# Kernel tuning notes

Measured on AMD Instinct MI355X. Metric: run time of the kernel, lower is better.

## Reference

```python
import jax, jax.numpy as jnp
import numpy as np

S_LEN, BATCH, D, HK, M, L, VOCAB = 1024, 4, 1024, 1024, 4096, 6, 32000
EPS = 1e-5


def layernorm(x, g, b):
    mu = x.mean(-1, keepdims=True)
    xc = x - mu
    var = (xc * xc).mean(-1, keepdims=True)
    return xc * jax.lax.rsqrt(var + EPS) * g + b


def block(z, wq, wk, wv, wc, g1, bb1, w1, b1, w2, b2, g2, bb2):
    # Faithful to the torch block: permute (1,0,2) at entry, never permute back.
    x = jnp.swapaxes(z, 0, 1)  # [B', S', d]
    d = x.shape[-1]
    Q = jnp.einsum('bsd,ed->bse', x, wq)
    K = jnp.einsum('bsd,ed->bse', x, wk)
    V = jnp.einsum('bsd,ed->bse', x, wv)
    # NOTE: scale is sqrt(embed_dim)=sqrt(d), not sqrt(k); no causal mask (faithful).
    scores = jnp.einsum('bse,bte->bst', Q, K) / jnp.sqrt(jnp.asarray(d, x.dtype))
    A = jax.nn.softmax(scores, axis=-1)
    ctx = jnp.einsum('bst,bte->bse', A, V)
    att = jnp.einsum('bse,de->bsd', ctx, wc) + x
    h = layernorm(att, g1, bb1)
    # NOTE: no nonlinearity in the FFN (faithful to the source).
    f = jnp.einsum('bsd,md->bsm', h, w1) + b1
    f = jnp.einsum('bsm,dm->bsd', f, w2) + b2
    return layernorm(f + h, g2, bb2)


def forward(x, word_emb, pos_emb, wq, wk, wv, wc, ln1_g, ln1_b, w1, b1, w2, b2,
            ln2_g, ln2_b, dec_w, dec_b, out_bias):
    S = x.shape[0]
    z = word_emb[x] * jnp.sqrt(jnp.asarray(D, word_emb.dtype))  # [S,B,d]
    z = jax.nn.relu(z + pos_emb[jnp.arange(S)][:, None, :])
    for i in range(L):  # small fixed layer count; shapes alternate layout so no scan
        z = block(z, wq[i], wk[i], wv[i], wc[i], ln1_g[i], ln1_b[i],
                  w1[i], b1[i], w2[i], b2[i], ln2_g[i], ln2_b[i])
    logits = jnp.einsum('sbd,vd->sbv', z, dec_w) + dec_b + out_bias
    return jax.nn.log_softmax(logits, axis=-1)


def setup_inputs() -> dict:
    key = jax.random.key(0)
    ks = jax.random.split(key, 16)
    std = jnp.float32(0.02)
    return {
        'x': jax.random.randint(ks[0], (S_LEN, BATCH), 0, VOCAB),
        'word_emb': jax.random.normal(ks[1], (VOCAB, D), jnp.float32) * std,
        'pos_emb': jax.random.normal(ks[2], (S_LEN, D), jnp.float32) * std,
        'wq': jax.random.normal(ks[3], (L, HK, D), jnp.float32) * std,
        'wk': jax.random.normal(ks[4], (L, HK, D), jnp.float32) * std,
        'wv': jax.random.normal(ks[5], (L, HK, D), jnp.float32) * std,
        'wc': jax.random.normal(ks[6], (L, D, HK), jnp.float32) * std,
        'ln1_g': jnp.ones((L, D), jnp.float32),
        'ln1_b': jnp.zeros((L, D), jnp.float32),
        'w1': jax.random.normal(ks[7], (L, M, D), jnp.float32) * std,
        'b1': jnp.zeros((L, M), jnp.float32),
        'w2': jax.random.normal(ks[8], (L, D, M), jnp.float32) * std,
        'b2': jnp.zeros((L, D), jnp.float32),
        'ln2_g': jnp.ones((L, D), jnp.float32),
        'ln2_b': jnp.zeros((L, D), jnp.float32),
        'dec_w': jax.random.normal(ks[9], (VOCAB, D), jnp.float32) * std,
        'dec_b': jnp.zeros((VOCAB,), jnp.float32),
        'out_bias': jnp.zeros((VOCAB,), jnp.float32),
    }


def reference(x, word_emb, pos_emb, wq, wk, wv, wc, ln1_g, ln1_b, w1, b1, w2, b2,
              ln2_g, ln2_b, dec_w, dec_b, out_bias):
    return forward(x, word_emb, pos_emb, wq, wk, wv, wc, ln1_g, ln1_b, w1, b1,
                   w2, b2, ln2_g, ln2_b, dec_w, dec_b, out_bias)
```

## Files before the change

### kernel.cpp

```cpp
#include <hip/hip_runtime.h>

typedef short short8 __attribute__((ext_vector_type(8)));
typedef float f32x4 __attribute__((ext_vector_type(4)));

#define DMODEL 1024
#define HKDIM 1024
#define MDIM 4096
#define NROW 4096
#define VOCAB 32000
#define NLAYER 6

#define GLOAD_LDS16(g, l)                                                      \
  __builtin_amdgcn_global_load_lds(                                            \
      (const __attribute__((address_space(1))) void*)(g),                      \
      (__attribute__((address_space(3))) void*)(l), 16, 0, 0)

__device__ __forceinline__ unsigned short f2bf(float f) {
  unsigned u = __float_as_uint(f);
  u += 0x7fffu + ((u >> 16) & 1u);
  return (unsigned short)(u >> 16);
}
__device__ __forceinline__ float bf2f(unsigned short h) {
  return __uint_as_float(((unsigned)h) << 16);
}
__device__ __forceinline__ float wave_sum(float v) {
  for (int o = 32; o; o >>= 1) v += __shfl_xor(v, o);
  return v;
}
__device__ __forceinline__ float wave_max(float v) {
  for (int o = 32; o; o >>= 1) v = fmaxf(v, __shfl_xor(v, o));
  return v;
}

__global__ __launch_bounds__(256) void k_embed(const int* __restrict__ x,
    const float* __restrict__ wemb, const float* __restrict__ pemb,
    float* __restrict__ z) {
  int r = blockIdx.x;
  int s = r >> 2;
  int tok = x[r];
  float4 a = ((const float4*)(wemb + (long)tok * DMODEL))[threadIdx.x];
  float4 p = ((const float4*)(pemb + (long)s * DMODEL))[threadIdx.x];
  float4 o;
  o.x = fmaxf(a.x * 32.0f + p.x, 0.0f);
  o.y = fmaxf(a.y * 32.0f + p.y, 0.0f);
  o.z = fmaxf(a.z * 32.0f + p.z, 0.0f);
  o.w = fmaxf(a.w * 32.0f + p.w, 0.0f);
  ((float4*)(z + (long)r * DMODEL))[threadIdx.x] = o;
}

__global__ __launch_bounds__(256) void k_permute(const float* __restrict__ zin,
    unsigned short* __restrict__ xb, int A0, int A1) {
  int r = blockIdx.x;
  int a1 = r / A0, a0 = r - a1 * A0;
  float4 v = ((const float4*)(zin + (long)(a0 * A1 + a1) * DMODEL))[threadIdx.x];
  ushort4 o = make_ushort4(f2bf(v.x), f2bf(v.y), f2bf(v.z), f2bf(v.w));
  ((ushort4*)(xb + (long)r * DMODEL))[threadIdx.x] = o;
}

__global__ __launch_bounds__(256) void k_cvt(const float* __restrict__ in,
    unsigned short* __restrict__ out, int n4) {
  int i = blockIdx.x * 256 + threadIdx.x;
  int stride = gridDim.x * 256;
  for (; i < n4; i += stride) {
    float4 v = ((const float4*)in)[i];
    ((ushort4*)out)[i] = make_ushort4(f2bf(v.x), f2bf(v.y), f2bf(v.z), f2bf(v.w));
  }
}

__global__ __launch_bounds__(256) void k_gemm_bt(
    const unsigned short* __restrict__ A, const unsigned short* __restrict__ B,
    float* __restrict__ Cf, unsigned short* __restrict__ Cb,
    const float* __restrict__ bias, const unsigned short* __restrict__ resb,
    int M, int N, int K, int lda, int ldb, int ldc,
    long aB, long bB, long cB, float scale) {
  __shared__ unsigned short As[128 * 64];
  __shared__ unsigned short Bs[128 * 64];
  const int tid = threadIdx.x;
  const int gx = gridDim.x, gy = gridDim.y;

  int nwg = gx * gy * gridDim.z;
  int flat = blockIdx.x + gx * (blockIdx.y + gy * blockIdx.z);
  int q8 = nwg >> 3, r8 = nwg & 7;
  int xcd = flat & 7, inner = flat >> 3;
  int wg = (xcd < r8 ? xcd * (q8 + 1) : r8 * (q8 + 1) + (xcd - r8) * q8) + inner;
  int ty = wg % gy;
  int rest = wg / gy;
  int tx = rest % gx;
  int tz = rest / gx;

  const unsigned short* Ab = A + (long)tz * aB;
  const unsigned short* Bb = B + (long)tz * bB;
  const int row0 = ty * 128, col0 = tx * 128;
  const int lane = tid & 63, w = tid >> 6;
  const int wm = w >> 1, wn = w & 1;
  const int fr = lane & 15, fg = lane >> 4, fr7 = fr & 7;
  const int lrow = lane >> 3;
  const int lcol = ((lane & 7) ^ lrow) * 8;

  const unsigned short* aSrc = Ab + (long)(row0 + w * 32 + lrow) * lda + lcol;
  const unsigned short* bSrc = Bb + (long)(col0 + w * 32 + lrow) * ldb + lcol;
  unsigned short* aDst = As + w * 32 * 64;
  unsigned short* bDst = Bs + w * 32 * 64;

  f32x4 acc[4][4];
#pragma unroll
  for (int i = 0; i < 4; ++i)
#pragma unroll
    for (int j = 0; j < 4; ++j)
#pragma unroll
      for (int qq = 0; qq < 4; ++qq) acc[i][j][qq] = 0.0f;

  for (int k0 = 0; k0 < K; k0 += 64) {
#pragma unroll
    for (int i = 0; i < 4; ++i) {
      GLOAD_LDS16(aSrc + (long)i * 8 * lda + k0, aDst + i * 512);
      GLOAD_LDS16(bSrc + (long)i * 8 * ldb + k0, bDst + i * 512);
    }
    __syncthreads();
#pragma unroll
    for (int kk = 0; kk < 64; kk += 32) {
      short8 af[4], bfr[4];
#pragma unroll
      for (int i = 0; i < 4; ++i) {
        af[i] = *(const short8*)(As + (wm * 64 + i * 16 + fr) * 64 +
                                 (((kk >> 3) + fg) ^ fr7) * 8);
        bfr[i] = *(const short8*)(Bs + (wn * 64 + i * 16 + fr) * 64 +
                                  (((kk >> 3) + fg) ^ fr7) * 8);
      }
#pragma unroll
      for (int i = 0; i < 4; ++i)
#pragma unroll
        for (int j = 0; j < 4; ++j)
          acc[i][j] = __builtin_amdgcn_mfma_f32_16x16x32_bf16(af[i], bfr[j], acc[i][j], 0, 0, 0);
    }
    __syncthreads();
  }

#pragma unroll
  for (int i = 0; i < 4; ++i) {
#pragma unroll
    for (int qq = 0; qq < 4; ++qq) {
      int row = row0 + wm * 64 + i * 16 + fg * 4 + qq;
#pragma unroll
      for (int j = 0; j < 4; ++j) {
        int col = col0 + wn * 64 + j * 16 + fr;
        long off = cB * tz + (long)row * ldc + col;
        float v = acc[i][j][qq] * scale + (bias ? bias[col] : 0.0f);
        if (resb) v += bf2f(resb[off]);
        if (Cf) Cf[off] = v;
        if (Cb) Cb[off] = f2bf(v);
      }
    }
  }
}

__global__ __launch_bounds__(256) void k_gemm64(
    const unsigned short* __restrict__ A, const unsigned short* __restrict__ B,
    float* __restrict__ Cf, unsigned short* __restrict__ Cb,
    const float* __restrict__ bias, const unsigned short* __restrict__ resb,
    int M, int N, int K, int lda, int ldb, int ldc,
    long aB, long bB, long cB, float scale) {
  __shared__ unsigned short As[64 * 64];
  __shared__ unsigned short Bs[128 * 64];
  const int tid = threadIdx.x;
  const int gx = gridDim.x, gy = gridDim.y;

  int nwg = gx * gy * gridDim.z;
  int flat = blockIdx.x + gx * (blockIdx.y + gy * blockIdx.z);
  int q8 = nwg >> 3, r8 = nwg & 7;
  int xcd = flat & 7, inner = flat >> 3;
  int wg = (xcd < r8 ? xcd * (q8 + 1) : r8 * (q8 + 1) + (xcd - r8) * q8) + inner;
  int ty = wg % gy;
  int rest = wg / gy;
  int tx = rest % gx;
  int tz = rest / gx;

  const unsigned short* Ab = A + (long)tz * aB;
  const unsigned short* Bb = B + (long)tz * bB;
  const int row0 = ty * 64, col0 = tx * 128;
  const int lane = tid & 63, w = tid >> 6;
  const int wm = w >> 1, wn = w & 1;
  const int fr = lane & 15, fg = lane >> 4, fr7 = fr & 7;
  const int lrow = lane >> 3;
  const int lcol = ((lane & 7) ^ lrow) * 8;

  const unsigned short* aSrc = Ab + (long)(row0 + w * 16 + lrow) * lda + lcol;
  const unsigned short* bSrc = Bb + (long)(col0 + w * 32 + lrow) * ldb + lcol;
  unsigned short* aDst = As + w * 16 * 64;
  unsigned short* bDst = Bs + w * 32 * 64;

  f32x4 acc[2][4];
#pragma unroll
  for (int i = 0; i < 2; ++i)
#pragma unroll
    for (int j = 0; j < 4; ++j)
#pragma unroll
      for (int qq = 0; qq < 4; ++qq) acc[i][j][qq] = 0.0f;

  for (int k0 = 0; k0 < K; k0 += 64) {
#pragma unroll
    for (int i = 0; i < 2; ++i)
      GLOAD_LDS16(aSrc + (long)i * 8 * lda + k0, aDst + i * 512);
#pragma unroll
    for (int i = 0; i < 4; ++i)
      GLOAD_LDS16(bSrc + (long)i * 8 * ldb + k0, bDst + i * 512);
    __syncthreads();
#pragma unroll
    for (int kk = 0; kk < 64; kk += 32) {
      short8 af[2], bfr[4];
#pragma unroll
      for (int i = 0; i < 2; ++i)
        af[i] = *(const short8*)(As + (wm * 32 + i * 16 + fr) * 64 +
                                 (((kk >> 3) + fg) ^ fr7) * 8);
#pragma unroll
      for (int j = 0; j < 4; ++j)
        bfr[j] = *(const short8*)(Bs + (wn * 64 + j * 16 + fr) * 64 +
                                  (((kk >> 3) + fg) ^ fr7) * 8);
#pragma unroll
      for (int i = 0; i < 2; ++i)
#pragma unroll
        for (int j = 0; j < 4; ++j)
          acc[i][j] = __builtin_amdgcn_mfma_f32_16x16x32_bf16(af[i], bfr[j], acc[i][j], 0, 0, 0);
    }
    __syncthreads();
  }

#pragma unroll
  for (int i = 0; i < 2; ++i) {
#pragma unroll
    for (int qq = 0; qq < 4; ++qq) {
      int row = row0 + wm * 32 + i * 16 + fg * 4 + qq;
#pragma unroll
      for (int j = 0; j < 4; ++j) {
        int col = col0 + wn * 64 + j * 16 + fr;
        long off = cB * tz + (long)row * ldc + col;
        float v = acc[i][j][qq] * scale + (bias ? bias[col] : 0.0f);
        if (resb) v += bf2f(resb[off]);
        if (Cf) Cf[off] = v;
        if (Cb) Cb[off] = f2bf(v);
      }
    }
  }
}

__global__ __launch_bounds__(512, 2) void k_gemm8(
    const unsigned short* __restrict__ A, const unsigned short* __restrict__ B,
    float* __restrict__ Cf, unsigned short* __restrict__ Cb,
    const float* __restrict__ bias, int M, int N, int K,
    int lda, int ldb, int ldc) {
  __shared__ unsigned short As[2][256 * 64];
  __shared__ unsigned short Bs[2][256 * 64];
  const int tid = threadIdx.x;
  const int gx = gridDim.x, gy = gridDim.y;
  int nwg = gx * gy;
  int flat = blockIdx.x + gx * blockIdx.y;
  int q8 = nwg >> 3, r8 = nwg & 7;
  int xcd = flat & 7, inner = flat >> 3;
  int wg = (xcd < r8 ? xcd * (q8 + 1) : r8 * (q8 + 1) + (xcd - r8) * q8) + inner;
  int ty = wg % gy, tx = wg / gy;

  const int row0 = ty * 256, col0 = tx * 256;
  const int lane = tid & 63, w = tid >> 6;
  const int wm = w >> 2, wn = w & 3;
  const int fr = lane & 15, fg = lane >> 4, fr7 = fr & 7;
  const int srow = lane >> 3;
  const int scol = ((lane & 7) ^ srow) * 8;

  const unsigned short* pA = A + (size_t)(row0 + w * 32 + srow) * lda + scol;
  const unsigned short* pB = B + (size_t)(col0 + w * 32 + srow) * ldb + scol;
  unsigned short* aD0 = &As[0][w * 32 * 64];
  unsigned short* bD0 = &Bs[0][w * 32 * 64];
  unsigned short* aD1 = &As[1][w * 32 * 64];
  unsigned short* bD1 = &Bs[1][w * 32 * 64];

  auto stage = [&](int bf, int tk) {
    unsigned short* aD = bf ? aD1 : aD0;
    unsigned short* bD = bf ? bD1 : bD0;
#pragma unroll
    for (int i = 0; i < 4; ++i) {
      GLOAD_LDS16(pA + (size_t)i * 8 * lda + (size_t)tk * 64, aD + i * 512);
      GLOAD_LDS16(pB + (size_t)i * 8 * ldb + (size_t)tk * 64, bD + i * 512);
    }
  };
  auto rdA = [&](const unsigned short* lds, int i, int kq) -> short8 {
    return *(const short8*)(lds + (wm * 128 + i * 16 + fr) * 64 +
                            (((kq << 2) + fg) ^ fr7) * 8);
  };
  auto rdB = [&](const unsigned short* lds, int j, int kq) -> short8 {
    return *(const short8*)(lds + (wn * 64 + j * 16 + fr) * 64 +
                            (((kq << 2) + fg) ^ fr7) * 8);
  };

  f32x4 acc[8][4];
#pragma unroll
  for (int i = 0; i < 8; ++i)
#pragma unroll
    for (int j = 0; j < 4; ++j)
#pragma unroll
      for (int qq = 0; qq < 4; ++qq) acc[i][j][qq] = 0.0f;

  const int NT = K >> 6;

  stage(0, 0);
  __syncthreads();

  for (int t = 0; t < NT; ++t) {
    const unsigned short* aL = (t & 1) ? &As[1][0] : &As[0][0];
    const unsigned short* bL = (t & 1) ? &Bs[1][0] : &Bs[0][0];
    if (t + 1 < NT) stage((t & 1) ^ 1, t + 1);
#pragma unroll
    for (int kq = 0; kq < 2; ++kq) {
      short8 a8[8], b8[4];
#pragma unroll
      for (int i = 0; i < 8; ++i) a8[i] = rdA(aL, i, kq);
#pragma unroll
      for (int j = 0; j < 4; ++j) b8[j] = rdB(bL, j, kq);
#pragma unroll
      for (int i = 0; i < 8; ++i)
#pragma unroll
        for (int j = 0; j < 4; ++j)
          acc[i][j] = __builtin_amdgcn_mfma_f32_16x16x32_bf16(a8[i], b8[j], acc[i][j], 0, 0, 0);
    }
    __syncthreads();
  }

#pragma unroll
  for (int i = 0; i < 8; ++i) {
#pragma unroll
    for (int qq = 0; qq < 4; ++qq) {
      int row = row0 + wm * 128 + i * 16 + fg * 4 + qq;
#pragma unroll
      for (int j = 0; j < 4; ++j) {
        int col = col0 + wn * 64 + j * 16 + fr;
        size_t off = (size_t)row * ldc + col;
        float v = acc[i][j][qq] + (bias ? bias[col] : 0.0f);
        if (Cf) Cf[off] = v;
        if (Cb) Cb[off] = f2bf(v);
      }
    }
  }
}

__global__ __launch_bounds__(256) void k_ln(const float* __restrict__ X,
    const unsigned short* __restrict__ X2b, const float* __restrict__ g,
    const float* __restrict__ b, float* __restrict__ outF,
    unsigned short* __restrict__ outB, int pA0, int pA1) {
  __shared__ float sm[4];
  int row = blockIdx.x, t = threadIdx.x;
  float4 v = ((const float4*)(X + (long)row * DMODEL))[t];
  if (X2b) {
    ushort4 u = ((const ushort4*)(X2b + (long)row * DMODEL))[t];
    v.x += bf2f(u.x); v.y += bf2f(u.y); v.z += bf2f(u.z); v.w += bf2f(u.w);
  }
  float s = wave_sum(v.x + v.y + v.z + v.w);
  if ((t & 63) == 0) sm[t >> 6] = s;
  __syncthreads();
  float mean = (sm[0] + sm[1] + sm[2] + sm[3]) * (1.0f / DMODEL);
  __syncthreads();
  float4 c;
  c.x = v.x - mean; c.y = v.y - mean; c.z = v.z - mean; c.w = v.w - mean;
  float ss = wave_sum(c.x * c.x + c.y * c.y + c.z * c.z + c.w * c.w);
  if ((t & 63) == 0) sm[t >> 6] = ss;
  __syncthreads();
  float var = (sm[0] + sm[1] + sm[2] + sm[3]) * (1.0f / DMODEL);
  float rs = rsqrtf(var + 1e-5f);
  float4 gv = ((const float4*)g)[t], bv = ((const float4*)b)[t];
  float4 o;
  o.x = c.x * rs * gv.x + bv.x;
  o.y = c.y * rs * gv.y + bv.y;
  o.z = c.z * rs * gv.z + bv.z;
  o.w = c.w * rs * gv.w + bv.w;
  if (outF) ((float4*)(outF + (long)row * DMODEL))[t] = o;
  if (outB) {
    int d = row;
    if (pA1 > 0) d = (row % pA1) * pA0 + row / pA1;
    ((ushort4*)(outB + (long)d * DMODEL))[t] =
        make_ushort4(f2bf(o.x), f2bf(o.y), f2bf(o.z), f2bf(o.w));
  }
}

__global__ __launch_bounds__(256) void k_softmax(const float* __restrict__ S,
    unsigned short* __restrict__ A) {
  __shared__ float sm[4];
  int row = blockIdx.x, t = threadIdx.x;
  float4 v = ((const float4*)(S + (long)row * 1024))[t];
  float m = wave_max(fmaxf(fmaxf(v.x, v.y), fmaxf(v.z, v.w)));
  if ((t & 63) == 0) sm[t >> 6] = m;
  __syncthreads();
  m = fmaxf(fmaxf(sm[0], sm[1]), fmaxf(sm[2], sm[3]));
  __syncthreads();
  float4 e;
  e.x = __expf(v.x - m); e.y = __expf(v.y - m);
  e.z = __expf(v.z - m); e.w = __expf(v.w - m);
  float s = wave_sum(e.x + e.y + e.z + e.w);
  if ((t & 63) == 0) sm[t >> 6] = s;
  __syncthreads();
  float inv = 1.0f / (sm[0] + sm[1] + sm[2] + sm[3]);
  ((ushort4*)(A + (long)row * 1024))[t] =
      make_ushort4(f2bf(e.x * inv), f2bf(e.y * inv), f2bf(e.z * inv), f2bf(e.w * inv));
}

__global__ __launch_bounds__(256) void k_attn4(const unsigned short* __restrict__ QKV,
    unsigned short* __restrict__ C) {
  int bp = blockIdx.x;
  int w = threadIdx.x >> 6, lane = threadIdx.x & 63;
  const unsigned short* q = QKV + (long)(bp * 4 + w) * 3072;
  float s[4];
  for (int j = 0; j < 4; ++j) {
    const unsigned short* kj = QKV + (long)(bp * 4 + j) * 3072 + 1024;
    float a = 0.0f;
    for (int e = lane; e < 1024; e += 64) a += bf2f(q[e]) * bf2f(kj[e]);
    s[j] = wave_sum(a) * (1.0f / 32.0f);
  }
  float m = fmaxf(fmaxf(s[0], s[1]), fmaxf(s[2], s[3]));
  float e0 = __expf(s[0] - m), e1 = __expf(s[1] - m);
  float e2 = __expf(s[2] - m), e3 = __expf(s[3] - m);
  float inv = 1.0f / (e0 + e1 + e2 + e3);
  float a0 = e0 * inv, a1 = e1 * inv, a2 = e2 * inv, a3 = e3 * inv;
  unsigned short* c = C + (long)(bp * 4 + w) * 1024;
  const unsigned short* v0 = QKV + (long)(bp * 4 + 0) * 3072 + 2048;
  const unsigned short* v1 = QKV + (long)(bp * 4 + 1) * 3072 + 2048;
  const unsigned short* v2 = QKV + (long)(bp * 4 + 2) * 3072 + 2048;
  const unsigned short* v3 = QKV + (long)(bp * 4 + 3) * 3072 + 2048;
  for (int e = lane; e < 1024; e += 64) {
    float v = a0 * bf2f(v0[e]) + a1 * bf2f(v1[e]) + a2 * bf2f(v2[e]) + a3 * bf2f(v3[e]);
    c[e] = f2bf(v);
  }
}

__global__ __launch_bounds__(256) void k_transpose(const unsigned short* __restrict__ in,
    unsigned short* __restrict__ out, int rows, int cols, int ld_in, int ld_out,
    long inB, long outB) {
  __shared__ unsigned short tile[32][33];
  long ibase = (long)blockIdx.z * inB;
  long obase = (long)blockIdx.z * outB;
  int r0 = blockIdx.y * 32, c0 = blockIdx.x * 32;
  int tx = threadIdx.x, ty = threadIdx.y;
  for (int i = ty; i < 32; i += 8)
    tile[i][tx] = in[ibase + (long)(r0 + i) * ld_in + c0 + tx];
  __syncthreads();
  for (int i = ty; i < 32; i += 8)
    out[obase + (long)(c0 + i) * ld_out + r0 + tx] = tile[tx][i];
}

__global__ __launch_bounds__(320) void k_logsoftmax_b(
    const unsigned short* __restrict__ Lb, float* __restrict__ out) {
  __shared__ float sm[5];
  int row = blockIdx.x, t = threadIdx.x;
  const unsigned long long* xr =
      (const unsigned long long*)(Lb + (long)row * VOCAB);
  float* yr = out + (long)row * VOCAB;
  float4 v[25];
  float m = -1e30f;
#pragma unroll
  for (int i = 0; i < 25; ++i) {
    unsigned long long u = __builtin_nontemporal_load(&xr[t + i * 320]);
    v[i].x = bf2f((unsigned short)(u & 0xffffu));
    v[i].y = bf2f((unsigned short)((u >> 16) & 0xffffu));
    v[i].z = bf2f((unsigned short)((u >> 32) & 0xffffu));
    v[i].w = bf2f((unsigned short)(u >> 48));
    m = fmaxf(m, fmaxf(fmaxf(v[i].x, v[i].y), fmaxf(v[i].z, v[i].w)));
  }
  m = wave_max(m);
  if ((t & 63) == 0) sm[t >> 6] = m;
  __syncthreads();
  m = fmaxf(fmaxf(fmaxf(sm[0], sm[1]), fmaxf(sm[2], sm[3])), sm[4]);
  __syncthreads();
  float s = 0.0f;
#pragma unroll
  for (int i = 0; i < 25; ++i)
    s += __expf(v[i].x - m) + __expf(v[i].y - m) + __expf(v[i].z - m) + __expf(v[i].w - m);
  s = wave_sum(s);
  if ((t & 63) == 0) sm[t >> 6] = s;
  __syncthreads();
  float l = m + __logf(sm[0] + sm[1] + sm[2] + sm[3] + sm[4]);
#pragma unroll
  for (int i = 0; i < 25; ++i) {
    float4 o = v[i];
    o.x -= l; o.y -= l; o.z -= l; o.w -= l;
    ((float4*)yr)[t + i * 320] = o;
  }
}

__global__ __launch_bounds__(320) void k_logsoftmax(float* __restrict__ L) {
  __shared__ float sm[5];
  int row = blockIdx.x, t = threadIdx.x;
  float* x = L + (long)row * VOCAB;
  float4 v[25];
  float m = -1e30f;
#pragma unroll
  for (int i = 0; i < 25; ++i) {
    v[i] = ((const float4*)x)[t + i * 320];
    m = fmaxf(m, fmaxf(fmaxf(v[i].x, v[i].y), fmaxf(v[i].z, v[i].w)));
  }
  m = wave_max(m);
  if ((t & 63) == 0) sm[t >> 6] = m;
  __syncthreads();
  m = fmaxf(fmaxf(fmaxf(sm[0], sm[1]), fmaxf(sm[2], sm[3])), sm[4]);
  __syncthreads();
  float s = 0.0f;
#pragma unroll
  for (int i = 0; i < 25; ++i)
    s += __expf(v[i].x - m) + __expf(v[i].y - m) + __expf(v[i].z - m) + __expf(v[i].w - m);
  s = wave_sum(s);
  if ((t & 63) == 0) sm[t >> 6] = s;
  __syncthreads();
  float l = m + __logf(sm[0] + sm[1] + sm[2] + sm[3] + sm[4]);
#pragma unroll
  for (int i = 0; i < 25; ++i) {
    float4 o = v[i];
    o.x -= l; o.y -= l; o.z -= l; o.w -= l;
    ((float4*)x)[t + i * 320] = o;
  }
}

__global__ __launch_bounds__(256) void k_addbias(const float* __restrict__ a,
    const float* __restrict__ b, float* __restrict__ o, int n) {
  int i = blockIdx.x * 256 + threadIdx.x;
  if (i < n) o[i] = a[i] + b[i];
}

extern "C" void kernel_launch(void* const* d_in, const int* in_sizes, int n_in,
                              void* d_out, int out_size, void* d_ws, size_t ws_size,
                              hipStream_t stream) {
  const int* x = (const int*)d_in[0];
  const float* wemb = (const float*)d_in[1];
  const float* pemb = (const float*)d_in[2];
  const float* wq = (const float*)d_in[3];
  const float* wk = (const float*)d_in[4];
  const float* wv = (const float*)d_in[5];
  const float* wc = (const float*)d_in[6];
  const float* ln1g = (const float*)d_in[7];
  const float* ln1b = (const float*)d_in[8];
  const float* w1 = (const float*)d_in[9];
  const float* b1 = (const float*)d_in[10];
  const float* w2 = (const float*)d_in[11];
  const float* b2 = (const float*)d_in[12];
  const float* ln2g = (const float*)d_in[13];
  const float* ln2b = (const float*)d_in[14];
  const float* decw = (const float*)d_in[15];
  const float* decb = (const float*)d_in[16];
  const float* obias = (const float*)d_in[17];
  float* out = (float*)d_out;

  char* ws = (char*)d_ws;
  size_t off = 0;
  auto alloc = [&](size_t bytes) -> char* {
    char* p = ws + off;
    off += (bytes + 255) & ~(size_t)255;
    return p;
  };
  float* z = (float*)alloc((size_t)NROW * DMODEL * 4);
  unsigned short* xb = (unsigned short*)alloc((size_t)NROW * DMODEL * 2);
  unsigned short* qkv = (unsigned short*)alloc((size_t)NROW * 3072 * 2);
  unsigned short* vt = (unsigned short*)alloc((size_t)NROW * HKDIM * 2);
  unsigned short* wbuf = (unsigned short*)alloc((size_t)MDIM * DMODEL * 2);
  float* tmp16 = (float*)alloc((size_t)NROW * 1024 * 4);
  unsigned short* am = (unsigned short*)alloc((size_t)NROW * 1024 * 2);
  unsigned short* ctx = (unsigned short*)alloc((size_t)NROW * HKDIM * 2);
  unsigned short* hb = (unsigned short*)alloc((size_t)NROW * DMODEL * 2);
  unsigned short* f = (unsigned short*)alloc((size_t)NROW * MDIM * 2);
  unsigned short* dwb = (unsigned short*)alloc((size_t)VOCAB * DMODEL * 2);
  unsigned short* zb = (unsigned short*)alloc((size_t)NROW * DMODEL * 2);
  float* biasD = (float*)alloc((size_t)VOCAB * 4);
  unsigned short* logits = (unsigned short*)alloc((size_t)NROW * VOCAB * 2);
  const bool bfLogits = (off <= ws_size);
  (void)in_sizes; (void)n_in; (void)out_size;

  auto gemm = [&](const unsigned short* A, const unsigned short* B, float* Cf,
                  unsigned short* Cb, const float* bias, const unsigned short* resb,
                  int M, int N, int K, int lda, int ldb, int ldc, int batch,
                  long aB, long bB, long cB, float scale) {
    dim3 g(N / 128, M / 128, batch);
    k_gemm_bt<<<g, dim3(256), 0, stream>>>(A, B, Cf, Cb, bias, resb, M, N, K,
                                           lda, ldb, ldc, aB, bB, cB, scale);
  };
  auto gemm64 = [&](const unsigned short* A, const unsigned short* B, float* Cf,
                    unsigned short* Cb, const float* bias, const unsigned short* resb,
                    int M, int N, int K, int lda, int ldb, int ldc, int batch,
                    long aB, long bB, long cB, float scale) {
    dim3 g(N / 128, M / 64, batch);
    k_gemm64<<<g, dim3(256), 0, stream>>>(A, B, Cf, Cb, bias, resb, M, N, K,
                                          lda, ldb, ldc, aB, bB, cB, scale);
  };
  auto gemm8 = [&](const unsigned short* A, const unsigned short* B, float* Cf,
                   unsigned short* Cb, const float* bias, int M, int N, int K,
                   int lda, int ldb, int ldc) {
    k_gemm8<<<dim3(N / 256, M / 256, 1), dim3(512), 0, stream>>>(
        A, B, Cf, Cb, bias, M, N, K, lda, ldb, ldc);
  };
  auto cvt = [&](const float* in, unsigned short* o, long n) {
    int n4 = (int)(n / 4);
    int grid = (n4 + 255) / 256;
    if (grid > 2048) grid = 2048;
    k_cvt<<<dim3(grid), dim3(256), 0, stream>>>(in, o, n4);
  };

  k_embed<<<NROW, 256, 0, stream>>>(x, wemb, pemb, z);
  k_permute<<<NROW, 256, 0, stream>>>(z, xb, 1024, 4);

  for (int i = 0; i < NLAYER; ++i) {
    int A0 = (i % 2 == 0) ? 1024 : 4;

    cvt(wq + (long)i * HKDIM * DMODEL, wbuf, (long)HKDIM * DMODEL);
    cvt(wk + (long)i * HKDIM * DMODEL, wbuf + (size_t)1024 * DMODEL, (long)HKDIM * DMODEL);
    cvt(wv + (long)i * HKDIM * DMODEL, wbuf + (size_t)2048 * DMODEL, (long)HKDIM * DMODEL);
    gemm(xb, wbuf, nullptr, qkv, nullptr, nullptr, NROW, 3072, DMODEL,
         DMODEL, DMODEL, 3072, 1, 0, 0, 0, 1.0f);

    if (A0 == 1024) {
      gemm64(qkv, qkv + 1024, tmp16, nullptr, nullptr, nullptr, 1024, 1024, 1024,
             3072, 3072, 1024, 4, (long)1024 * 3072, (long)1024 * 3072, 1 << 20,
             1.0f / 32.0f);
      k_softmax<<<NROW, 256, 0, stream>>>(tmp16, am);
      k_transpose<<<dim3(32, 32, 4), dim3(32, 8), 0, stream>>>(
          qkv + 2048, vt, 1024, 1024, 3072, 1024, (long)1024 * 3072, 1 << 20);
      gemm64(am, vt, nullptr, ctx, nullptr, nullptr, 1024, 1024, 1024,
             1024, 1024, 1024, 4, 1 << 20, 1 << 20, 1 << 20, 1.0f);
    } else {
      k_attn4<<<1024, 256, 0, stream>>>(qkv, ctx);
    }

    cvt(wc + (long)i * DMODEL * HKDIM, wbuf, (long)DMODEL * HKDIM);
    gemm64(ctx, wbuf, tmp16, nullptr, nullptr, xb, NROW, DMODEL, HKDIM,
           HKDIM, HKDIM, DMODEL, 1, 0, 0, 0, 1.0f);
    k_ln<<<NROW, 256, 0, stream>>>(tmp16, nullptr, ln1g + (long)i * DMODEL,
                                   ln1b + (long)i * DMODEL, nullptr, hb, 0, 0);
    cvt(w1 + (long)i * MDIM * DMODEL, wbuf, (long)MDIM * DMODEL);
    gemm(hb, wbuf, nullptr, f, b1 + (long)i * MDIM, nullptr, NROW, MDIM, DMODEL,
         DMODEL, DMODEL, MDIM, 1, 0, 0, 0, 1.0f);
    cvt(w2 + (long)i * DMODEL * MDIM, wbuf, (long)DMODEL * MDIM);
    gemm64(f, wbuf, tmp16, nullptr, b2 + (long)i * DMODEL, nullptr, NROW, DMODEL, MDIM,
           MDIM, MDIM, DMODEL, 1, 0, 0, 0, 1.0f);
    if (i == NLAYER - 1) {
      k_ln<<<NROW, 256, 0, stream>>>(tmp16, hb, ln2g + (long)i * DMODEL,
                                     ln2b + (long)i * DMODEL, nullptr, zb, 0, 0);
    } else {
      int A0n = ((i + 1) % 2 == 0) ? 1024 : 4;
      int A1n = 4096 / A0n;
      k_ln<<<NROW, 256, 0, stream>>>(tmp16, hb, ln2g + (long)i * DMODEL,
                                     ln2b + (long)i * DMODEL, nullptr, xb, A0n, A1n);
    }
  }

  cvt(decw, dwb, (long)VOCAB * DMODEL);
  k_addbias<<<(VOCAB + 255) / 256, 256, 0, stream>>>(decb, obias, biasD, VOCAB);
  if (bfLogits) {
    gemm8(zb, dwb, nullptr, logits, biasD, NROW, VOCAB, DMODEL, DMODEL, DMODEL, VOCAB);
    k_logsoftmax_b<<<NROW, 320, 0, stream>>>(logits, out);
  } else {
    gemm8(zb, dwb, out, nullptr, biasD, NROW, VOCAB, DMODEL, DMODEL, DMODEL, VOCAB);
    k_logsoftmax<<<NROW, 320, 0, stream>>>(out);
  }
}
```

Before: 2.197 ms.

## Pipeline 256x256 GEMM into quarter-tile stages and use it for FFN1

Rewrites the 256x256 bf16 GEMM so each K-step is split into four MFMA quadrants. Global-to-LDS loads for the next tiles are issued piecewise between them, with explicit vmcnt/lgkmcnt waits, barriers and setprio raised around the MFMA bursts. This aims to overlap memory traffic with matrix math instead of staging a whole tile and then syncing once per step. The same kernel also replaces the 128x128 GEMM for the first FFN projection. The extra barriers and hand-placed waits add synchronization overhead and correctness risk around buffer reuse.

```diff
diff --git a/kernel.cpp b/kernel.cpp
--- a/kernel.cpp
+++ b/kernel.cpp
@@ -243,7 +243,7 @@
   }
 }
 
-__global__ __launch_bounds__(512, 2) void k_gemm8(
+__global__ __launch_bounds__(512, 2) void k_gemm8p(
     const unsigned short* __restrict__ A, const unsigned short* __restrict__ B,
     float* __restrict__ Cf, unsigned short* __restrict__ Cb,
     const float* __restrict__ bias, int M, int N, int K,
@@ -265,23 +265,20 @@
   const int fr = lane & 15, fg = lane >> 4, fr7 = fr & 7;
   const int srow = lane >> 3;
   const int scol = ((lane & 7) ^ srow) * 8;
-
-  const unsigned short* pA = A + (size_t)(row0 + w * 32 + srow) * lda + scol;
-  const unsigned short* pB = B + (size_t)(col0 + w * 32 + srow) * ldb + scol;
-  unsigned short* aD0 = &As[0][w * 32 * 64];
-  unsigned short* bD0 = &Bs[0][w * 32 * 64];
-  unsigned short* aD1 = &As[1][w * 32 * 64];
-  unsigned short* bD1 = &Bs[1][w * 32 * 64];
-
-  auto stage = [&](int bf, int tk) {
-    unsigned short* aD = bf ? aD1 : aD0;
-    unsigned short* bD = bf ? bD1 : bD0;
-#pragma unroll
-    for (int i = 0; i < 4; ++i) {
-      GLOAD_LDS16(pA + (size_t)i * 8 * lda + (size_t)tk * 64, aD + i * 512);
-      GLOAD_LDS16(pB + (size_t)i * 8 * ldb + (size_t)tk * 64, bD + i * 512);
-    }
+  const int bq = (w >> 1) * 64 + (w & 1) * 16;
+
+  const unsigned short* pA = A + (size_t)(row0 + srow) * lda + scol;
+  const unsigned short* pB = B + (size_t)(col0 + srow) * ldb + scol;
+
+  auto stg = [&](const unsigned short* base, int ld, int tk,
+                 unsigned short* lds, int r0) {
+    GLOAD_LDS16(base + (size_t)r0 * ld + (size_t)tk * 64, lds + r0 * 64);
   };
+#define STALO(bf, tk) { stg(pA, lda, tk, &As[bf][0], w * 8); stg(pA, lda, tk, &As[bf][0], 128 + w * 8); }
+#define STAHI(bf, tk) { stg(pA, lda, tk, &As[bf][0], 64 + w * 8); stg(pA, lda, tk, &As[bf][0], 192 + w * 8); }
+#define STB01(bf, tk) { stg(pB, ldb, tk, &Bs[bf][0], bq); stg(pB, ldb, tk, &Bs[bf][0], bq + 8); }
+#define STB23(bf, tk) { stg(pB, ldb, tk, &Bs[bf][0], bq + 32); stg(pB, ldb, tk, &Bs[bf][0], bq + 40); }
+
   auto rdA = [&](const unsigned short* lds, int i, int kq) -> short8 {
     return *(const short8*)(lds + (wm * 128 + i * 16 + fr) * 64 +
                             (((kq << 2) + fg) ^ fr7) * 8);
@@ -299,30 +296,75 @@
 #pragma unroll
       for (int qq = 0; qq < 4; ++qq) acc[i][j][qq] = 0.0f;
 
+  short8 a8[8], b01[4], b23[4];
+
+#define MFMA16(I0, BR, J0)                                                   \
+  {                                                                          \
+    __builtin_amdgcn_s_setprio(1);                                           \
+    _Pragma("unroll") for (int kq = 0; kq < 2; ++kq)                         \
+      _Pragma("unroll") for (int i = 0; i < 4; ++i)                          \
+        _Pragma("unroll") for (int j = 0; j < 2; ++j)                        \
+          acc[(I0) + i][(J0) + j] = __builtin_amdgcn_mfma_f32_16x16x32_bf16( \
+              a8[i * 2 + kq], BR[j * 2 + kq], acc[(I0) + i][(J0) + j], 0, 0, 0); \
+    __builtin_amdgcn_s_setprio(0);                                           \
+  }
+
   const int NT = K >> 6;
 
-  stage(0, 0);
-  __syncthreads();
+  STALO(0, 0) STAHI(0, 0) STB01(0, 0) STB23(0, 0)
+  STALO(1, 1) STB01(1, 1) STB23(1, 1)
+  asm volatile("s_waitcnt vmcnt(6)" ::: "memory");
+  __builtin_amdgcn_s_barrier();
 
   for (int t = 0; t < NT; ++t) {
-    const unsigned short* aL = (t & 1) ? &As[1][0] : &As[0][0];
-    const unsigned short* bL = (t & 1) ? &Bs[1][0] : &Bs[0][0];
-    if (t + 1 < NT) stage((t & 1) ^ 1, t + 1);
-#pragma unroll
-    for (int kq = 0; kq < 2; ++kq) {
-      short8 a8[8], b8[4];
-#pragma unroll
-      for (int i = 0; i < 8; ++i) a8[i] = rdA(aL, i, kq);
-#pragma unroll
-      for (int j = 0; j < 4; ++j) b8[j] = rdB(bL, j, kq);
-#pragma unroll
-      for (int i = 0; i < 8; ++i)
-#pragma unroll
-        for (int j = 0; j < 4; ++j)
-          acc[i][j] = __builtin_amdgcn_mfma_f32_16x16x32_bf16(a8[i], b8[j], acc[i][j], 0, 0, 0);
-    }
-    __syncthreads();
-  }
+    const int b = t & 1;
+    const unsigned short* aL = &As[b][0];
+    const unsigned short* bL = &Bs[b][0];
+    const int tp1 = (t + 1 < NT) ? t + 1 : NT - 1;
+    const int tp2 = (t + 2 < NT) ? t + 2 : NT - 1;
+#pragma unroll
+    for (int i = 0; i < 4; ++i) {
+      a8[i * 2] = rdA(aL, i, 0);
+      a8[i * 2 + 1] = rdA(aL, i, 1);
+    }
+#pragma unroll
+    for (int j = 0; j < 2; ++j) {
+      b01[j * 2] = rdB(bL, j, 0);
+      b01[j * 2 + 1] = rdB(bL, j, 1);
+    }
+    STAHI(1 - b, tp1)
+    asm volatile("s_waitcnt lgkmcnt(8)" ::: "memory");
+    __builtin_amdgcn_s_barrier();
+    asm volatile("s_waitcnt lgkmcnt(0)" ::: "memory");
+    MFMA16(0, b01, 0)
+    __builtin_amdgcn_s_barrier();
+#pragma unroll
+    for (int j = 0; j < 2; ++j) {
+      b23[j * 2] = rdB(bL, j + 2, 0);
+      b23[j * 2 + 1] = rdB(bL, j + 2, 1);
+    }
+    STALO(b, tp2)
+    __builtin_amdgcn_s_barrier();
+    asm volatile("s_waitcnt lgkmcnt(0)" ::: "memory");
+    MFMA16(0, b23, 2)
+    __builtin_amdgcn_s_barrier();
+#pragma unroll
+    for (int i = 0; i < 4; ++i) {
+      a8[i * 2] = rdA(aL, i + 4, 0);
+      a8[i * 2 + 1] = rdA(aL, i + 4, 1);
+    }
+    STB01(b, tp2)
+    __builtin_amdgcn_s_barrier();
+    asm volatile("s_waitcnt lgkmcnt(0)" ::: "memory");
+    MFMA16(4, b23, 2)
+    __builtin_amdgcn_s_barrier();
+    STB23(b, tp2)
+    __builtin_amdgcn_s_barrier();
+    MFMA16(4, b01, 0)
+    asm volatile("s_waitcnt vmcnt(6)" ::: "memory");
+    __builtin_amdgcn_s_barrier();
+  }
+  asm volatile("s_waitcnt vmcnt(0)" ::: "memory");
 
 #pragma unroll
   for (int i = 0; i < 8; ++i) {
@@ -339,6 +381,11 @@
       }
     }
   }
+#undef STALO
+#undef STAHI
+#undef STB01
+#undef STB23
+#undef MFMA16
 }
 
 __global__ __launch_bounds__(256) void k_ln(const float* __restrict__ X,
@@ -583,10 +630,10 @@
     k_gemm64<<<g, dim3(256), 0, stream>>>(A, B, Cf, Cb, bias, resb, M, N, K,
                                           lda, ldb, ldc, aB, bB, cB, scale);
   };
-  auto gemm8 = [&](const unsigned short* A, const unsigned short* B, float* Cf,
-                   unsigned short* Cb, const float* bias, int M, int N, int K,
-                   int lda, int ldb, int ldc) {
-    k_gemm8<<<dim3(N / 256, M / 256, 1), dim3(512), 0, stream>>>(
+  auto gemm8p = [&](const unsigned short* A, const unsigned short* B, float* Cf,
+                    unsigned short* Cb, const float* bias, int M, int N, int K,
+                    int lda, int ldb, int ldc) {
+    k_gemm8p<<<dim3(N / 256, M / 256, 1), dim3(512), 0, stream>>>(
         A, B, Cf, Cb, bias, M, N, K, lda, ldb, ldc);
   };
   auto cvt = [&](const float* in, unsigned short* o, long n) {
@@ -627,8 +674,8 @@
     k_ln<<<NROW, 256, 0, stream>>>(tmp16, nullptr, ln1g + (long)i * DMODEL,
                                    ln1b + (long)i * DMODEL, nullptr, hb, 0, 0);
     cvt(w1 + (long)i * MDIM * DMODEL, wbuf, (long)MDIM * DMODEL);
-    gemm(hb, wbuf, nullptr, f, b1 + (long)i * MDIM, nullptr, NROW, MDIM, DMODEL,
-         DMODEL, DMODEL, MDIM, 1, 0, 0, 0, 1.0f);
+    gemm8p(hb, wbuf, nullptr, f, b1 + (long)i * MDIM, NROW, MDIM, DMODEL,
+           DMODEL, DMODEL, MDIM);
     cvt(w2 + (long)i * DMODEL * MDIM, wbuf, (long)DMODEL * MDIM);
     gemm64(f, wbuf, tmp16, nullptr, b2 + (long)i * DMODEL, nullptr, NROW, DMODEL, MDIM,
            MDIM, MDIM, DMODEL, 1, 0, 0, 0, 1.0f);
@@ -646,10 +693,10 @@
   cvt(decw, dwb, (long)VOCAB * DMODEL);
   k_addbias<<<(VOCAB + 255) / 256, 256, 0, stream>>>(decb, obias, biasD, VOCAB);
   if (bfLogits) {
-    gemm8(zb, dwb, nullptr, logits, biasD, NROW, VOCAB, DMODEL, DMODEL, DMODEL, VOCAB);
+    gemm8p(zb, dwb, nullptr, logits, biasD, NROW, VOCAB, DMODEL, DMODEL, DMODEL, VOCAB);
     k_logsoftmax_b<<<NROW, 320, 0, stream>>>(logits, out);
   } else {
-    gemm8(zb, dwb, out, nullptr, biasD, NROW, VOCAB, DMODEL, DMODEL, DMODEL, VOCAB);
+    gemm8p(zb, dwb, out, nullptr, biasD, NROW, VOCAB, DMODEL, DMODEL, DMODEL, VOCAB);
     k_logsoftmax<<<NROW, 320, 0, stream>>>(out);
   }
 }
```

Measured after the change: 2.193 ms. About the same (-0.2%).
